# Optimization experiments

Hardware: AMD Instinct MI355X
Metric: run time of the kernel (lower is better)

## Reference

```python
import jax, jax.numpy as jnp
import numpy as np

SLOPE = 0.1  # LeakyReLU negative slope

def _inv_sqrt(v):
    # pow(v, -0.5) with inf -> 0 (matches torch isinf masking)
    return jnp.where(v > 0, v ** -0.5, 0.0)

def setup_inputs() -> dict:
    key = jax.random.key(0)
    ks = jax.random.split(key, 5)
    P, D, I, H, R = 2048, 4096, 512, 256, 5
    return {
        "p_feat": jax.random.normal(ks[0], (P, I), dtype=jnp.float32),
        "d_feat": jax.random.normal(ks[1], (D, I), dtype=jnp.float32),
        "p": jnp.arange(P, dtype=jnp.int64),
        "d": jnp.arange(D, dtype=jnp.int64),
        "support": jax.random.uniform(ks[2], (R, P, D), dtype=jnp.float32),
        "p_weight": jax.random.normal(ks[3], (R, I, H), dtype=jnp.float32) * (6.0 / (I + H)) ** 0.5,
        "p_bias": jax.random.normal(ks[4], (H,), dtype=jnp.float32),
    }

def reference(p_feat, d_feat, p, d, support, p_weight, p_bias):
    # dropout p=0.0 -> identity (eval semantics)
    # cumulative weight sum across relations: w_cum[r] = sum_{r'<=r} p_weight[r']
    w_cum = jnp.cumsum(p_weight, axis=0)                 # [R, I, H]
    tmp_p = jnp.einsum('pi,rih->rph', p_feat, w_cum)     # [R, P, H]
    tmp_d = jnp.einsum('di,rih->rdh', d_feat, w_cum)     # [R, D, H]

    # normalize(S) = diag(colsum(S)^-1/2) @ S @ diag(rowsum_axis0(S)^-1/2)
    # (torch code builds NxN diags + matmuls; equivalent to broadcast scaling)
    col_scale = _inv_sqrt(support.sum(axis=1))           # [R, D] (sum over P)
    row_scale = _inv_sqrt(support.sum(axis=2))           # [R, P] (sum over D)
    norm = support * row_scale[:, :, None] * col_scale[:, None, :]  # [R, P, D]
    # note: normalize(S.T) == normalize(S).T, so reuse norm for the drug side

    z_p = jnp.einsum('rpd,rdh->ph', norm[:, p, :], tmp_d)   # gather protein rows
    z_d = jnp.einsum('rpd,rph->dh', norm[:, :, d], tmp_p)   # gather drug rows of S.T
    z_p = z_p + p_bias
    z_d = z_d + p_bias  # d_bias is tied to p_bias

    leaky = lambda x: jnp.where(x >= 0, x, SLOPE * x)
    return (leaky(z_p), leaky(z_d))
```

## Files before the change

kernel.cpp:

```cpp
#include <hip/hip_runtime.h>

typedef __bf16 bf16x8 __attribute__((ext_vector_type(8)));
typedef __bf16 bf16x4 __attribute__((ext_vector_type(4)));
typedef float  f32x4  __attribute__((ext_vector_type(4)));

#define P_  2048
#define D_  4096
#define IC_ 512
#define H_  256
#define R_  5
#define KP_ (R_*D_)
#define KD_ (R_*P_)

__device__ __forceinline__ int swzf(int row){ return ((row>>1) ^ (row>>3)) & 3; }

__device__ __forceinline__ bf16x8 cvt8(float4 a, float4 b){
  bf16x8 o;
  o[0]=(__bf16)a.x; o[1]=(__bf16)a.y; o[2]=(__bf16)a.z; o[3]=(__bf16)a.w;
  o[4]=(__bf16)b.x; o[5]=(__bf16)b.y; o[6]=(__bf16)b.z; o[7]=(__bf16)b.w;
  return o;
}

__device__ __forceinline__ void gl_lds16(const __bf16* g, __bf16* l){
  __builtin_amdgcn_global_load_lds(
    (const __attribute__((address_space(1))) unsigned int*)(g),
    (__attribute__((address_space(3))) unsigned int*)(l), 16, 0, 0);
}

__global__ __launch_bounds__(256) void k_prep2(const float* __restrict__ S,
    const float* __restrict__ pw, __bf16* __restrict__ Sbf, float* __restrict__ rs,
    float* __restrict__ cspart, __bf16* __restrict__ wct){
  __shared__ float wsum[32][4];
  const int t = threadIdx.x;
  if (blockIdx.x >= 320){
    const int h  = t;
    const int i0 = (blockIdx.x - 320) * 8;
    float acc[8];
    #pragma unroll
    for (int j=0;j<8;++j) acc[j]=0.f;
    for (int r=0;r<R_;++r){
      bf16x8 o;
      #pragma unroll
      for (int j=0;j<8;++j){
        acc[j] += pw[((size_t)r*IC_ + i0 + j)*H_ + h];
        o[j] = (__bf16)acc[j];
      }
      *reinterpret_cast<bf16x8*>(wct + ((size_t)r*H_ + h)*IC_ + i0) = o;
    }
    return;
  }
  const int lane = t & 63, w = t >> 6;
  const int slab = blockIdx.x;
  const int r = slab >> 6, z = slab & 63;
  const size_t row0 = (size_t)r*P_ + (size_t)z*32;
  const float4* src = reinterpret_cast<const float4*>(S + row0*D_);
  __bf16* dst = Sbf + row0*D_;
  f32x4 ca[4];
  #pragma unroll
  for (int c=0;c<4;++c){ ca[c][0]=0.f; ca[c][1]=0.f; ca[c][2]=0.f; ca[c][3]=0.f; }
  for (int pp=0; pp<32; ++pp){
    float4 v[4];
    #pragma unroll
    for (int c=0;c<4;++c) v[c] = src[(size_t)pp*(D_/4) + t + 256*c];
    float rsum = 0.f;
    #pragma unroll
    for (int c=0;c<4;++c){
      ca[c][0]+=v[c].x; ca[c][1]+=v[c].y; ca[c][2]+=v[c].z; ca[c][3]+=v[c].w;
      rsum += v[c].x+v[c].y+v[c].z+v[c].w;
      bf16x4 o; o[0]=(__bf16)v[c].x; o[1]=(__bf16)v[c].y; o[2]=(__bf16)v[c].z; o[3]=(__bf16)v[c].w;
      *reinterpret_cast<bf16x4*>(dst + (size_t)pp*D_ + (t + 256*c)*4) = o;
    }
    #pragma unroll
    for (int off = 32; off; off >>= 1) rsum += __shfl_xor(rsum, off);
    if (lane == 0) wsum[pp][w] = rsum;
  }
  __syncthreads();
  if (t < 32){
    float s = wsum[t][0]+wsum[t][1]+wsum[t][2]+wsum[t][3];
    rs[row0 + t] = (s > 0.f) ? rsqrtf(s) : 0.f;
  }
  float* o = cspart + ((size_t)z*R_ + r)*D_;
  #pragma unroll
  for (int c=0;c<4;++c) *reinterpret_cast<f32x4*>(o + (t + 256*c)*4) = ca[c];
}

__global__ void k_csfin(const float* __restrict__ cspart, float* __restrict__ cs){
  const int i = blockIdx.x*256 + threadIdx.x;
  float s = 0.f;
  #pragma unroll
  for (int z = 0; z < 64; ++z) s += cspart[(size_t)z*(R_*D_) + i];
  cs[i] = (s > 0.f) ? rsqrtf(s) : 0.f;
}

__global__ __launch_bounds__(256) void k_tmp(const float* __restrict__ p_feat,
    const float* __restrict__ d_feat, const float* __restrict__ rs,
    const float* __restrict__ cs, const __bf16* __restrict__ wct,
    __bf16* __restrict__ Tpt, __bf16* __restrict__ Tdt){
  __shared__ __bf16 As[64*40];
  const int t = threadIdx.x, lane = t & 63, w = t >> 6;
  const int mt = blockIdx.x, r = blockIdx.y;
  const bool isp = mt < (P_/64);
  const float* feat  = isp ? p_feat : d_feat;
  const float* scale = isp ? rs : cs;
  __bf16* outT = isp ? Tpt : Tdt;
  const int M  = isp ? P_ : D_;
  const int RM = isp ? KD_ : KP_;
  const int m0 = (isp ? mt : mt - P_/64)*64;
  const int srow = t >> 2, skc = (t & 3)*8;
  f32x4 acc[4][4];
  #pragma unroll
  for (int a=0;a<4;++a)
    #pragma unroll
    for (int b=0;b<4;++b){ acc[a][b][0]=0.f; acc[a][b][1]=0.f; acc[a][b][2]=0.f; acc[a][b][3]=0.f; }

  for (int ks = 0; ks < IC_; ks += 32){
    __syncthreads();
    {
      const float* g = feat + (size_t)(m0+srow)*IC_ + ks + skc;
      float4 a = *(const float4*)g, b = *(const float4*)(g+4);
      *reinterpret_cast<bf16x8*>(&As[srow*40 + skc]) = cvt8(a,b);
    }
    __syncthreads();
    bf16x8 af[4], bfv[4];
    #pragma unroll
    for (int tt=0;tt<4;++tt)
      af[tt] = *reinterpret_cast<const bf16x8*>(&As[(16*tt + (lane&15))*40 + (lane>>4)*8]);
    #pragma unroll
    for (int cc=0;cc<4;++cc)
      bfv[cc] = *reinterpret_cast<const bf16x8*>(wct + ((size_t)r*H_ + w*64 + 16*cc + (lane&15))*IC_ + ks + (lane>>4)*8);
    #pragma unroll
    for (int tt=0;tt<4;++tt)
      #pragma unroll
      for (int cc=0;cc<4;++cc)
        acc[tt][cc] = __builtin_amdgcn_mfma_f32_16x16x32_bf16(af[tt], bfv[cc], acc[tt][cc], 0, 0, 0);
  }
  #pragma unroll
  for (int tt=0;tt<4;++tt){
    const int mb = m0 + 16*tt + ((lane>>4)<<2);
    const float s0 = scale[r*M+mb+0], s1 = scale[r*M+mb+1],
                s2 = scale[r*M+mb+2], s3 = scale[r*M+mb+3];
    #pragma unroll
    for (int cc=0;cc<4;++cc){
      const int hc = (w<<6) + 16*cc + (lane&15);
      bf16x4 v;
      v[0]=(__bf16)(acc[tt][cc][0]*s0); v[1]=(__bf16)(acc[tt][cc][1]*s1);
      v[2]=(__bf16)(acc[tt][cc][2]*s2); v[3]=(__bf16)(acc[tt][cc][3]*s3);
      *reinterpret_cast<bf16x4*>(outT + (size_t)hc*RM + r*M + mb) = v;
    }
  }
}

__global__ __launch_bounds__(512, 4) void k_z(const __bf16* __restrict__ Sbf,
    const __bf16* __restrict__ Tdt, const __bf16* __restrict__ Tpt,
    float* __restrict__ partP, float* __restrict__ partD){
  __shared__ __bf16 As[128*32];
  __shared__ __bf16 Bs[256*32];
  const int t = threadIdx.x, lane = t & 63, w = t >> 6;
  const int wm = w >> 2, wn = w & 3;
  const int bid = blockIdx.x;
  const bool isp = bid < 320;
  const int tile  = isp ? (bid & 15) : ((bid-320) & 31);
  const int split = isp ? (bid >> 4) : ((bid-320) >> 5);
  const int m0 = tile*128;
  const int kbase = split*1024;
  const __bf16* Bsrc = isp ? Tdt : Tpt;
  const int bstr = isp ? KP_ : KD_;
  const int arow = t >> 2;
  const int akо = ((t & 3) ^ swzf(arow)) * 8;
  const int prow = t >> 4, d8 = (t & 15)*8;
  const int kqw = prow >> 3, koff = prow & 7;
  const int brow0 = t >> 2, brow1 = 128 + brow0;
  const int bko0 = ((t & 3) ^ swzf(brow0)) * 8;
  const int bko1 = ((t & 3) ^ swzf(brow1)) * 8;
  f32x4 acc[4][4];
  #pragma unroll
  for (int a=0;a<4;++a)
    #pragma unroll
    for (int b=0;b<4;++b){ acc[a][b][0]=0.f; acc[a][b][1]=0.f; acc[a][b][2]=0.f; acc[a][b][3]=0.f; }

  for (int ko = 0; ko < 1024; ko += 32){
    const int kg = kbase + ko;
    __syncthreads();
    if (isp){
      const int r = kg >> 12, dd = kg & (D_-1);
      gl_lds16(Sbf + ((size_t)r*P_ + m0 + arow)*D_ + dd + akо, As + w*512);
    } else {
      const int r = kg >> 11, pp = kg & (P_-1);
      bf16x8 va = *reinterpret_cast<const bf16x8*>(Sbf + ((size_t)r*P_ + pp + prow)*D_ + m0 + d8);
      #pragma unroll
      for (int j=0;j<8;++j){
        const int rowd = d8 + j;
        As[rowd*32 + ((kqw ^ swzf(rowd))<<3) + koff] = va[j];
      }
    }
    gl_lds16(Bsrc + (size_t)brow0*bstr + kg + bko0, Bs + w*512);
    gl_lds16(Bsrc + (size_t)brow1*bstr + kg + bko1, Bs + 4096 + w*512);
    __syncthreads();
    const int kq = lane >> 4;
    bf16x8 bv[4];
    #pragma unroll
    for (int cc=0;cc<4;++cc){
      const int row = wn*64 + 16*cc + (lane&15);
      bv[cc] = *reinterpret_cast<const bf16x8*>(&Bs[row*32 + ((kq ^ swzf(row))<<3)]);
    }
    #pragma unroll
    for (int tt=0;tt<4;++tt){
      const int row = wm*64 + 16*tt + (lane&15);
      bf16x8 af = *reinterpret_cast<const bf16x8*>(&As[row*32 + ((kq ^ swzf(row))<<3)]);
      #pragma unroll
      for (int cc=0;cc<4;++cc)
        acc[tt][cc] = __builtin_amdgcn_mfma_f32_16x16x32_bf16(af, bv[cc], acc[tt][cc], 0, 0, 0);
    }
  }
  float* o = isp ? (partP + (size_t)split*((size_t)P_*H_))
                 : (partD + (size_t)split*((size_t)D_*H_));
  #pragma unroll
  for (int tt=0;tt<4;++tt){
    const int mb = m0 + wm*64 + 16*tt + ((lane>>4)<<2);
    #pragma unroll
    for (int cc=0;cc<4;++cc){
      const int hc = wn*64 + 16*cc + (lane&15);
      #pragma unroll
      for (int j=0;j<4;++j) o[(size_t)(mb+j)*H_ + hc] = acc[tt][cc][j];
    }
  }
}

__global__ void k_reduce(const float* __restrict__ partP, const float* __restrict__ partD,
    const float* __restrict__ rs, const float* __restrict__ cs,
    const float* __restrict__ bias, float* __restrict__ out){
  const int i = (blockIdx.x*256 + threadIdx.x)*4;
  float4 s; s.x=s.y=s.z=s.w=0.f;
  if (i < P_*H_){
    const int p = i >> 8;
    #pragma unroll
    for (int z = 0; z < 20; ++z){
      const float sc = rs[(z>>2)*P_ + p];
      float4 v = *(const float4*)(partP + (size_t)z*((size_t)P_*H_) + i);
      s.x+=sc*v.x; s.y+=sc*v.y; s.z+=sc*v.z; s.w+=sc*v.w;
    }
  } else {
    const int j = i - P_*H_;
    const int d = j >> 8;
    #pragma unroll
    for (int z = 0; z < 10; ++z){
      const float sc = cs[(z>>1)*D_ + d];
      float4 v = *(const float4*)(partD + (size_t)z*((size_t)D_*H_) + j);
      s.x+=sc*v.x; s.y+=sc*v.y; s.z+=sc*v.z; s.w+=sc*v.w;
    }
  }
  const float4 b = *(const float4*)(bias + (i & (H_-1)));
  s.x+=b.x; s.y+=b.y; s.z+=b.z; s.w+=b.w;
  s.x = (s.x>=0.f)? s.x : 0.1f*s.x;
  s.y = (s.y>=0.f)? s.y : 0.1f*s.y;
  s.z = (s.z>=0.f)? s.z : 0.1f*s.z;
  s.w = (s.w>=0.f)? s.w : 0.1f*s.w;
  *(float4*)(out + i) = s;
}

extern "C" void kernel_launch(void* const* d_in, const int* in_sizes, int n_in,
                              void* d_out, int out_size, void* d_ws, size_t ws_size,
                              hipStream_t stream){
  (void)in_sizes; (void)n_in; (void)out_size; (void)ws_size;
  const float* p_feat = (const float*)d_in[0];
  const float* d_feat = (const float*)d_in[1];
  const float* S      = (const float*)d_in[4];
  const float* pw     = (const float*)d_in[5];
  const float* bias   = (const float*)d_in[6];
  float* out = (float*)d_out;

  char* ws = (char*)d_ws;
  __bf16* wct    = (__bf16*)(ws + 0);
  __bf16* Tdt    = (__bf16*)(ws + 1310720);
  __bf16* Tpt    = (__bf16*)(ws + 11796480);
  float*  rs     = (float*) (ws + 17039360);
  float*  cs     = (float*) (ws + 17080320);
  float*  cspart = (float*) (ws + 17162240);
  __bf16* Sbf    = (__bf16*)(ws + 22405120);
  float*  partP  = (float*) (ws + 106291200);
  float*  partD  = (float*) (ws + 148234240);

  k_prep2 <<<384, 256, 0, stream>>>(S, pw, Sbf, rs, cspart, wct);
  k_csfin <<<(R_*D_)/256, 256, 0, stream>>>(cspart, cs);
  k_tmp   <<<dim3((P_+D_)/64, R_), 256, 0, stream>>>(p_feat, d_feat, rs, cs, wct, Tpt, Tdt);
  k_z     <<<640, 512, 0, stream>>>(Sbf, Tdt, Tpt, partP, partD);
  k_reduce<<<((P_+D_)*H_)/1024, 256, 0, stream>>>(partP, partD, rs, cs, bias, out);
}
```

Measured before the change: 211.3 us.

## Deepen GEMM K-tile, fold row/col scaling into A loads, cut split-K partials

The z-GEMM now uses a K tile of 64 with an 8-way XOR swizzle and runs two MFMA sub-steps per barrier pair, which halves the number of synchronisations. The rs/cs normalisation scale is applied to S while it is staged into LDS rather than in the reduction. The split-K factor drops from 20/10 to 16/8 (512 blocks instead of 640), so there are fewer partial buffers to write and the reduce only sums them. In exchange the A path for protein tiles moves from async global_load_lds to register loads plus scaling, the kernel uses more LDS, and rounding the scaled S to bf16 adds a little error.

```diff
diff --git a/kernel.cpp b/kernel.cpp
--- a/kernel.cpp
+++ b/kernel.cpp
@@ -12,6 +12,7 @@
 #define KP_ (R_*D_)
 #define KD_ (R_*P_)
 
+__device__ __forceinline__ int swz8(int row){ return (row ^ (row>>3)) & 7; }
 __device__ __forceinline__ int swzf(int row){ return ((row>>1) ^ (row>>3)) & 3; }
 
 __device__ __forceinline__ bf16x8 cvt8(float4 a, float4 b){
@@ -151,65 +152,85 @@
 }
 
 __global__ __launch_bounds__(512, 4) void k_z(const __bf16* __restrict__ Sbf,
+    const float* __restrict__ rs, const float* __restrict__ cs,
     const __bf16* __restrict__ Tdt, const __bf16* __restrict__ Tpt,
     float* __restrict__ partP, float* __restrict__ partD){
-  __shared__ __bf16 As[128*32];
-  __shared__ __bf16 Bs[256*32];
+  __shared__ __bf16 As[128*64];
+  __shared__ __bf16 Bs[256*64];
   const int t = threadIdx.x, lane = t & 63, w = t >> 6;
   const int wm = w >> 2, wn = w & 3;
   const int bid = blockIdx.x;
-  const bool isp = bid < 320;
-  const int tile  = isp ? (bid & 15) : ((bid-320) & 31);
-  const int split = isp ? (bid >> 4) : ((bid-320) >> 5);
+  const bool isp = bid < 256;
+  const int tile  = isp ? (bid & 15) : ((bid-256) & 31);
+  const int split = isp ? (bid >> 4) : ((bid-256) >> 5);
   const int m0 = tile*128;
-  const int kbase = split*1024;
+  const int kbase = split*1280;
   const __bf16* Bsrc = isp ? Tdt : Tpt;
   const int bstr = isp ? KP_ : KD_;
-  const int arow = t >> 2;
-  const int akо = ((t & 3) ^ swzf(arow)) * 8;
-  const int prow = t >> 4, d8 = (t & 15)*8;
-  const int kqw = prow >> 3, koff = prow & 7;
-  const int brow0 = t >> 2, brow1 = 128 + brow0;
-  const int bko0 = ((t & 3) ^ swzf(brow0)) * 8;
-  const int bko1 = ((t & 3) ^ swzf(brow1)) * 8;
+  const int srow = t >> 3, sslot = t & 7;
+  const int krow0 = t >> 4, d8 = (t & 15)*8;
   f32x4 acc[4][4];
   #pragma unroll
   for (int a=0;a<4;++a)
     #pragma unroll
     for (int b=0;b<4;++b){ acc[a][b][0]=0.f; acc[a][b][1]=0.f; acc[a][b][2]=0.f; acc[a][b][3]=0.f; }
 
-  for (int ko = 0; ko < 1024; ko += 32){
+  for (int ko = 0; ko < 1280; ko += 64){
     const int kg = kbase + ko;
     __syncthreads();
     if (isp){
       const int r = kg >> 12, dd = kg & (D_-1);
-      gl_lds16(Sbf + ((size_t)r*P_ + m0 + arow)*D_ + dd + akо, As + w*512);
+      #pragma unroll
+      for (int q=0;q<2;++q){
+        const int row = q*64 + srow;
+        const float sc = rs[r*P_ + m0 + row];
+        bf16x8 v = *reinterpret_cast<const bf16x8*>(Sbf + ((size_t)r*P_ + m0 + row)*D_ + dd + sslot*8);
+        bf16x8 o;
+        #pragma unroll
+        for (int j=0;j<8;++j) o[j] = (__bf16)((float)v[j] * sc);
+        *reinterpret_cast<bf16x8*>(&As[row*64 + ((sslot ^ swz8(row))<<3)]) = o;
+      }
     } else {
       const int r = kg >> 11, pp = kg & (P_-1);
-      bf16x8 va = *reinterpret_cast<const bf16x8*>(Sbf + ((size_t)r*P_ + pp + prow)*D_ + m0 + d8);
-      #pragma unroll
-      for (int j=0;j<8;++j){
-        const int rowd = d8 + j;
-        As[rowd*32 + ((kqw ^ swzf(rowd))<<3) + koff] = va[j];
-      }
-    }
-    gl_lds16(Bsrc + (size_t)brow0*bstr + kg + bko0, Bs + w*512);
-    gl_lds16(Bsrc + (size_t)brow1*bstr + kg + bko1, Bs + 4096 + w*512);
+      const float4 c1 = *(const float4*)(cs + r*D_ + m0 + d8);
+      const float4 c2 = *(const float4*)(cs + r*D_ + m0 + d8 + 4);
+      float cf[8] = {c1.x,c1.y,c1.z,c1.w,c2.x,c2.y,c2.z,c2.w};
+      #pragma unroll
+      for (int q=0;q<2;++q){
+        const int kr = q*32 + krow0;
+        bf16x8 va = *reinterpret_cast<const bf16x8*>(Sbf + ((size_t)r*P_ + pp + kr)*D_ + m0 + d8);
+        const int slot = kr >> 3, kb = kr & 7;
+        #pragma unroll
+        for (int j=0;j<8;++j){
+          const int rowd = d8 + j;
+          As[rowd*64 + ((slot ^ swz8(rowd))<<3) + kb] = (__bf16)((float)va[j] * cf[j]);
+        }
+      }
+    }
+    #pragma unroll
+    for (int q=0;q<4;++q){
+      const int row = q*64 + srow;
+      gl_lds16(Bsrc + (size_t)row*bstr + kg + ((sslot ^ swz8(row))<<3), Bs + q*4096 + w*512);
+    }
     __syncthreads();
     const int kq = lane >> 4;
-    bf16x8 bv[4];
-    #pragma unroll
-    for (int cc=0;cc<4;++cc){
-      const int row = wn*64 + 16*cc + (lane&15);
-      bv[cc] = *reinterpret_cast<const bf16x8*>(&Bs[row*32 + ((kq ^ swzf(row))<<3)]);
-    }
-    #pragma unroll
-    for (int tt=0;tt<4;++tt){
-      const int row = wm*64 + 16*tt + (lane&15);
-      bf16x8 af = *reinterpret_cast<const bf16x8*>(&As[row*32 + ((kq ^ swzf(row))<<3)]);
-      #pragma unroll
-      for (int cc=0;cc<4;++cc)
-        acc[tt][cc] = __builtin_amdgcn_mfma_f32_16x16x32_bf16(af, bv[cc], acc[tt][cc], 0, 0, 0);
+    #pragma unroll
+    for (int ksub=0; ksub<2; ++ksub){
+      const int s = ksub*4 + kq;
+      bf16x8 bv[4];
+      #pragma unroll
+      for (int cc=0;cc<4;++cc){
+        const int row = wn*64 + 16*cc + (lane&15);
+        bv[cc] = *reinterpret_cast<const bf16x8*>(&Bs[row*64 + ((s ^ swz8(row))<<3)]);
+      }
+      #pragma unroll
+      for (int tt=0;tt<4;++tt){
+        const int row = wm*64 + 16*tt + (lane&15);
+        bf16x8 af = *reinterpret_cast<const bf16x8*>(&As[row*64 + ((s ^ swz8(row))<<3)]);
+        #pragma unroll
+        for (int cc=0;cc<4;++cc)
+          acc[tt][cc] = __builtin_amdgcn_mfma_f32_16x16x32_bf16(af, bv[cc], acc[tt][cc], 0, 0, 0);
+      }
     }
   }
   float* o = isp ? (partP + (size_t)split*((size_t)P_*H_))
@@ -227,26 +248,21 @@
 }
 
 __global__ void k_reduce(const float* __restrict__ partP, const float* __restrict__ partD,
-    const float* __restrict__ rs, const float* __restrict__ cs,
     const float* __restrict__ bias, float* __restrict__ out){
   const int i = (blockIdx.x*256 + threadIdx.x)*4;
   float4 s; s.x=s.y=s.z=s.w=0.f;
   if (i < P_*H_){
-    const int p = i >> 8;
-    #pragma unroll
-    for (int z = 0; z < 20; ++z){
-      const float sc = rs[(z>>2)*P_ + p];
+    #pragma unroll
+    for (int z = 0; z < 16; ++z){
       float4 v = *(const float4*)(partP + (size_t)z*((size_t)P_*H_) + i);
-      s.x+=sc*v.x; s.y+=sc*v.y; s.z+=sc*v.z; s.w+=sc*v.w;
+      s.x+=v.x; s.y+=v.y; s.z+=v.z; s.w+=v.w;
     }
   } else {
     const int j = i - P_*H_;
-    const int d = j >> 8;
-    #pragma unroll
-    for (int z = 0; z < 10; ++z){
-      const float sc = cs[(z>>1)*D_ + d];
+    #pragma unroll
+    for (int z = 0; z < 8; ++z){
       float4 v = *(const float4*)(partD + (size_t)z*((size_t)D_*H_) + j);
-      s.x+=sc*v.x; s.y+=sc*v.y; s.z+=sc*v.z; s.w+=sc*v.w;
+      s.x+=v.x; s.y+=v.y; s.z+=v.z; s.w+=v.w;
     }
   }
   const float4 b = *(const float4*)(bias + (i & (H_-1)));
@@ -278,11 +294,11 @@
   float*  cspart = (float*) (ws + 17162240);
   __bf16* Sbf    = (__bf16*)(ws + 22405120);
   float*  partP  = (float*) (ws + 106291200);
-  float*  partD  = (float*) (ws + 148234240);
+  float*  partD  = (float*) (ws + 139845632);
 
   k_prep2 <<<384, 256, 0, stream>>>(S, pw, Sbf, rs, cspart, wct);
   k_csfin <<<(R_*D_)/256, 256, 0, stream>>>(cspart, cs);
   k_tmp   <<<dim3((P_+D_)/64, R_), 256, 0, stream>>>(p_feat, d_feat, rs, cs, wct, Tpt, Tdt);
-  k_z     <<<640, 512, 0, stream>>>(Sbf, Tdt, Tpt, partP, partD);
-  k_reduce<<<((P_+D_)*H_)/1024, 256, 0, stream>>>(partP, partD, rs, cs, bias, out);
-}
+  k_z     <<<512, 512, 0, stream>>>(Sbf, rs, cs, Tdt, Tpt, partP, partD);
+  k_reduce<<<((P_+D_)*H_)/1024, 256, 0, stream>>>(partP, partD, bias, out);
+}
```

Result: slower. 218.0 us (+3.2%).

## Double-buffer k_z LDS tiles, fold row/col scales into A, and cut split-K count

Applied to the files above, without the earlier changes.

The GEMM kernel gets double-buffered LDS with register prefetch of the A tile two steps ahead, so global loads overlap the MFMA work on the current buffer. The per-relation rs/cs scale is now applied while A is written to LDS, which lets the reduce kernel do a plain sum. Split-K goes from 1024- to 1280-wide chunks, giving 512 blocks instead of 640 and fewer partials to write and reduce. The cost is more LDS per block, register-staged A loads in place of direct-to-LDS loads on the protein side, and a wait count that must match the loads actually in flight.

```diff
diff --git a/kernel.cpp b/kernel.cpp
--- a/kernel.cpp
+++ b/kernel.cpp
@@ -150,68 +150,118 @@
   }
 }
 
+#define KG_(j) (kbase + 32*(j))
+#define LOADA_(j, dst) { const int kg_ = KG_(j); \
+  if (isp){ const int r_ = kg_>>12, dd_ = kg_&(D_-1); \
+    dst = *reinterpret_cast<const bf16x8*>(Sbf + ((size_t)r_*P_ + m0 + arow)*D_ + dd_ + (t&3)*8); } \
+  else { const int r_ = kg_>>11, pp_ = kg_&(P_-1); \
+    dst = *reinterpret_cast<const bf16x8*>(Sbf + ((size_t)r_*P_ + pp_ + prow)*D_ + m0 + d8); } }
+
+#define WRITEA_(j, va, Ab) { const int kg_ = KG_(j); \
+  if (isp){ const int r_ = kg_>>12; const float sc_ = (r_==rA) ? scA : scB; \
+    bf16x8 o_; \
+    _Pragma("unroll") for (int jj=0;jj<8;++jj) o_[jj] = (__bf16)((float)va[jj]*sc_); \
+    *reinterpret_cast<bf16x8*>(&(Ab)[arow*32 + aslot*8]) = o_; } \
+  else { const int r_ = kg_>>11; const bool uA_ = (r_==rA); \
+    _Pragma("unroll") for (int jj=0;jj<8;++jj){ const int rowd_ = d8 + jj; \
+      (Ab)[rowd_*32 + ((kqw ^ swzf(rowd_))<<3) + koff] = (__bf16)((float)va[jj]*(uA_?cAf[jj]:cBf[jj])); } } }
+
+#define ISSUEB_(j, Bb) { const int kg_ = KG_(j); \
+  gl_lds16(Bsrc + (size_t)brow0*bstr + kg_ + bko0, (Bb) + w*512); \
+  gl_lds16(Bsrc + (size_t)brow1*bstr + kg_ + bko1, (Bb) + 4096 + w*512); }
+
 __global__ __launch_bounds__(512, 4) void k_z(const __bf16* __restrict__ Sbf,
+    const float* __restrict__ rs, const float* __restrict__ cs,
     const __bf16* __restrict__ Tdt, const __bf16* __restrict__ Tpt,
     float* __restrict__ partP, float* __restrict__ partD){
-  __shared__ __bf16 As[128*32];
-  __shared__ __bf16 Bs[256*32];
+  __shared__ __bf16 As[2][128*32];
+  __shared__ __bf16 Bs[2][256*32];
   const int t = threadIdx.x, lane = t & 63, w = t >> 6;
   const int wm = w >> 2, wn = w & 3;
   const int bid = blockIdx.x;
-  const bool isp = bid < 320;
-  const int tile  = isp ? (bid & 15) : ((bid-320) & 31);
-  const int split = isp ? (bid >> 4) : ((bid-320) >> 5);
+  const bool isp = bid < 256;
+  const int tile  = isp ? (bid & 15) : ((bid-256) & 31);
+  const int split = isp ? (bid >> 4) : ((bid-256) >> 5);
   const int m0 = tile*128;
-  const int kbase = split*1024;
+  const int kbase = split*1280;
   const __bf16* Bsrc = isp ? Tdt : Tpt;
   const int bstr = isp ? KP_ : KD_;
-  const int arow = t >> 2;
-  const int akо = ((t & 3) ^ swzf(arow)) * 8;
+  const int arow  = t >> 2;
+  const int aslot = (t & 3) ^ swzf(arow);
   const int prow = t >> 4, d8 = (t & 15)*8;
   const int kqw = prow >> 3, koff = prow & 7;
   const int brow0 = t >> 2, brow1 = 128 + brow0;
   const int bko0 = ((t & 3) ^ swzf(brow0)) * 8;
   const int bko1 = ((t & 3) ^ swzf(brow1)) * 8;
+
+  const int rA = isp ? (kbase >> 12) : (kbase >> 11);
+  const int rB = isp ? ((kbase+1279) >> 12) : ((kbase+1279) >> 11);
+  float scA = 0.f, scB = 0.f;
+  float cAf[8], cBf[8];
+  if (isp){
+    scA = rs[rA*P_ + m0 + arow];
+    scB = rs[rB*P_ + m0 + arow];
+  } else {
+    float4 a1 = *(const float4*)(cs + rA*D_ + m0 + d8);
+    float4 a2 = *(const float4*)(cs + rA*D_ + m0 + d8 + 4);
+    float4 b1 = *(const float4*)(cs + rB*D_ + m0 + d8);
+    float4 b2 = *(const float4*)(cs + rB*D_ + m0 + d8 + 4);
+    cAf[0]=a1.x; cAf[1]=a1.y; cAf[2]=a1.z; cAf[3]=a1.w;
+    cAf[4]=a2.x; cAf[5]=a2.y; cAf[6]=a2.z; cAf[7]=a2.w;
+    cBf[0]=b1.x; cBf[1]=b1.y; cBf[2]=b1.z; cBf[3]=b1.w;
+    cBf[4]=b2.x; cBf[5]=b2.y; cBf[6]=b2.z; cBf[7]=b2.w;
+  }
+
   f32x4 acc[4][4];
   #pragma unroll
   for (int a=0;a<4;++a)
     #pragma unroll
     for (int b=0;b<4;++b){ acc[a][b][0]=0.f; acc[a][b][1]=0.f; acc[a][b][2]=0.f; acc[a][b][3]=0.f; }
 
-  for (int ko = 0; ko < 1024; ko += 32){
-    const int kg = kbase + ko;
-    __syncthreads();
-    if (isp){
-      const int r = kg >> 12, dd = kg & (D_-1);
-      gl_lds16(Sbf + ((size_t)r*P_ + m0 + arow)*D_ + dd + akо, As + w*512);
-    } else {
-      const int r = kg >> 11, pp = kg & (P_-1);
-      bf16x8 va = *reinterpret_cast<const bf16x8*>(Sbf + ((size_t)r*P_ + pp + prow)*D_ + m0 + d8);
-      #pragma unroll
-      for (int j=0;j<8;++j){
-        const int rowd = d8 + j;
-        As[rowd*32 + ((kqw ^ swzf(rowd))<<3) + koff] = va[j];
-      }
-    }
-    gl_lds16(Bsrc + (size_t)brow0*bstr + kg + bko0, Bs + w*512);
-    gl_lds16(Bsrc + (size_t)brow1*bstr + kg + bko1, Bs + 4096 + w*512);
-    __syncthreads();
+  {
+    bf16x8 v0, v1;
+    LOADA_(0, v0);
+    LOADA_(1, v1);
+    WRITEA_(0, v0, As[0]);
+    ISSUEB_(0, Bs[0]);
+    WRITEA_(1, v1, As[1]);
+    ISSUEB_(1, Bs[1]);
+  }
+  bf16x8 vhold;
+  LOADA_(2, vhold);
+
+  for (int i = 0; i < 40; ++i){
+    __bf16* Ac = As[i & 1];
+    __bf16* Bc = Bs[i & 1];
+    asm volatile("s_waitcnt vmcnt(3) lgkmcnt(0)" ::: "memory");
+    __builtin_amdgcn_s_barrier();
+    __builtin_amdgcn_sched_barrier(0);
     const int kq = lane >> 4;
     bf16x8 bv[4];
     #pragma unroll
     for (int cc=0;cc<4;++cc){
       const int row = wn*64 + 16*cc + (lane&15);
-      bv[cc] = *reinterpret_cast<const bf16x8*>(&Bs[row*32 + ((kq ^ swzf(row))<<3)]);
+      bv[cc] = *reinterpret_cast<const bf16x8*>(&Bc[row*32 + ((kq ^ swzf(row))<<3)]);
     }
     #pragma unroll
     for (int tt=0;tt<4;++tt){
       const int row = wm*64 + 16*tt + (lane&15);
-      bf16x8 af = *reinterpret_cast<const bf16x8*>(&As[row*32 + ((kq ^ swzf(row))<<3)]);
+      bf16x8 af = *reinterpret_cast<const bf16x8*>(&Ac[row*32 + ((kq ^ swzf(row))<<3)]);
       #pragma unroll
       for (int cc=0;cc<4;++cc)
         acc[tt][cc] = __builtin_amdgcn_mfma_f32_16x16x32_bf16(af, bv[cc], acc[tt][cc], 0, 0, 0);
     }
-  }
+    __builtin_amdgcn_sched_barrier(0);
+    __builtin_amdgcn_s_barrier();
+    const int j2 = (i+2 > 39) ? 39 : (i+2);
+    const int j3 = (i+3 > 39) ? 39 : (i+3);
+    bf16x8 vtmp;
+    LOADA_(j3, vtmp);
+    WRITEA_(j2, vhold, Ac);
+    ISSUEB_(j2, Bc);
+    vhold = vtmp;
+  }
+
   float* o = isp ? (partP + (size_t)split*((size_t)P_*H_))
                  : (partD + (size_t)split*((size_t)D_*H_));
   #pragma unroll
@@ -227,26 +277,21 @@
 }
 
 __global__ void k_reduce(const float* __restrict__ partP, const float* __restrict__ partD,
-    const float* __restrict__ rs, const float* __restrict__ cs,
     const float* __restrict__ bias, float* __restrict__ out){
   const int i = (blockIdx.x*256 + threadIdx.x)*4;
   float4 s; s.x=s.y=s.z=s.w=0.f;
   if (i < P_*H_){
-    const int p = i >> 8;
-    #pragma unroll
-    for (int z = 0; z < 20; ++z){
-      const float sc = rs[(z>>2)*P_ + p];
+    #pragma unroll
+    for (int z = 0; z < 16; ++z){
       float4 v = *(const float4*)(partP + (size_t)z*((size_t)P_*H_) + i);
-      s.x+=sc*v.x; s.y+=sc*v.y; s.z+=sc*v.z; s.w+=sc*v.w;
+      s.x+=v.x; s.y+=v.y; s.z+=v.z; s.w+=v.w;
     }
   } else {
     const int j = i - P_*H_;
-    const int d = j >> 8;
-    #pragma unroll
-    for (int z = 0; z < 10; ++z){
-      const float sc = cs[(z>>1)*D_ + d];
+    #pragma unroll
+    for (int z = 0; z < 8; ++z){
       float4 v = *(const float4*)(partD + (size_t)z*((size_t)D_*H_) + j);
-      s.x+=sc*v.x; s.y+=sc*v.y; s.z+=sc*v.z; s.w+=sc*v.w;
+      s.x+=v.x; s.y+=v.y; s.z+=v.z; s.w+=v.w;
     }
   }
   const float4 b = *(const float4*)(bias + (i & (H_-1)));
@@ -278,11 +323,11 @@
   float*  cspart = (float*) (ws + 17162240);
   __bf16* Sbf    = (__bf16*)(ws + 22405120);
   float*  partP  = (float*) (ws + 106291200);
-  float*  partD  = (float*) (ws + 148234240);
+  float*  partD  = (float*) (ws + 139845632);
 
   k_prep2 <<<384, 256, 0, stream>>>(S, pw, Sbf, rs, cspart, wct);
   k_csfin <<<(R_*D_)/256, 256, 0, stream>>>(cspart, cs);
   k_tmp   <<<dim3((P_+D_)/64, R_), 256, 0, stream>>>(p_feat, d_feat, rs, cs, wct, Tpt, Tdt);
-  k_z     <<<640, 512, 0, stream>>>(Sbf, Tdt, Tpt, partP, partD);
-  k_reduce<<<((P_+D_)*H_)/1024, 256, 0, stream>>>(partP, partD, rs, cs, bias, out);
-}
+  k_z     <<<512, 512, 0, stream>>>(Sbf, rs, cs, Tdt, Tpt, partP, partD);
+  k_reduce<<<((P_+D_)*H_)/1024, 256, 0, stream>>>(partP, partD, bias, out);
+}
```

Measured after the change: 211.2 us. Within noise of the previous version (-0.0%).
